# Performance work log

Measured on AMD Instinct MI355X. Metric: run time of the kernel, lower is better.

## Reference

```python
import jax, jax.numpy as jnp
import numpy as np

C, H_HEADS, L_LEV, M_PTS = 256, 4, 3, 4
TAU0 = 1.0


def _ln(x, g, b, eps=1e-5):
    mu = x.mean(-1, keepdims=True)
    var = ((x - mu) ** 2).mean(-1, keepdims=True)
    return (x - mu) * jax.lax.rsqrt(var + eps) * g + b


def _grid_sample(v, grid):
    """Bilinear grid_sample, padding_mode='zeros', align_corners=True.
    v: [B,C,Hin,Win], grid: [B,N,2] (x,y) in [-1,1] -> [B,N,C]"""
    B, Cc, Hin, Win = v.shape
    x = (grid[..., 0] + 1.0) * 0.5 * (Win - 1)
    y = (grid[..., 1] + 1.0) * 0.5 * (Hin - 1)
    x0 = jnp.floor(x); y0 = jnp.floor(y)
    wx1 = x - x0; wy1 = y - y0
    x0i = x0.astype(jnp.int32); y0i = y0.astype(jnp.int32)
    vflat = v.reshape(B, Cc, Hin * Win).transpose(0, 2, 1)  # [B,HW,C]

    def tap(yi, xi, w):
        valid = ((xi >= 0) & (xi < Win) & (yi >= 0) & (yi < Hin)).astype(v.dtype)
        idx = jnp.clip(yi, 0, Hin - 1) * Win + jnp.clip(xi, 0, Win - 1)  # [B,N]
        g = jax.vmap(lambda vf, i: vf[i])(vflat, idx)  # [B,N,C]
        return g * (w * valid)[..., None]

    return (tap(y0i, x0i, (1 - wy1) * (1 - wx1))
            + tap(y0i, x0i + 1, (1 - wy1) * wx1)
            + tap(y0i + 1, x0i, wy1 * (1 - wx1))
            + tap(y0i + 1, x0i + 1, wy1 * wx1))


def setup_inputs() -> dict:
    key = jax.random.key(0)
    ks = jax.random.split(key, 32)
    B, Hq, Wq = 2, 64, 64
    cins = [256, 512, 1024]
    d = {
        'S':  jax.random.normal(ks[0], (B, C, Hq, Wq), jnp.float32),
        'f0': jax.random.normal(ks[1], (B, cins[0], 64, 64), jnp.float32),
        'f1': jax.random.normal(ks[2], (B, cins[1], 32, 32), jnp.float32),
        'f2': jax.random.normal(ks[3], (B, cins[2], 16, 16), jnp.float32),
        'sim': jax.random.uniform(ks[4], (B, 1, Hq, Wq), jnp.float32),
        # 1x1 conv value projections per level
        'vw0': jax.random.normal(ks[5], (C, cins[0]), jnp.float32) * 0.02,
        'vb0': jnp.zeros((C,), jnp.float32),
        'vw1': jax.random.normal(ks[6], (C, cins[1]), jnp.float32) * 0.02,
        'vb1': jnp.zeros((C,), jnp.float32),
        'vw2': jax.random.normal(ks[7], (C, cins[2]), jnp.float32) * 0.02,
        'vb2': jnp.zeros((C,), jnp.float32),
        'q_w': jax.random.normal(ks[8], (C, C), jnp.float32) * 0.02,
        'q_b': jnp.zeros((C,), jnp.float32),
        # offset/weight predictors (non-zero so sampling is nontrivial)
        'off_w': jax.random.normal(ks[9], (H_HEADS * L_LEV * M_PTS * 2, C), jnp.float32) * 0.01,
        'off_b': jnp.zeros((H_HEADS * L_LEV * M_PTS * 2,), jnp.float32),
        'wgt_w': jax.random.normal(ks[10], (H_HEADS * L_LEV * M_PTS, C), jnp.float32) * 0.02,
        'wgt_b': jnp.zeros((H_HEADS * L_LEV * M_PTS,), jnp.float32),
        'out_w': jax.random.normal(ks[11], (C, H_HEADS * C), jnp.float32) * 0.02,
        'out_b': jnp.zeros((C,), jnp.float32),
        'lnq_g': jnp.ones((C,), jnp.float32), 'lnq_b': jnp.zeros((C,), jnp.float32),
        'lno_g': jnp.ones((C,), jnp.float32), 'lno_b': jnp.zeros((C,), jnp.float32),
        'fc1_w': jax.random.normal(ks[12], (4 * C, C), jnp.float32) * 0.02,
        'fc1_b': jnp.zeros((4 * C,), jnp.float32),
        'fc2_w': jax.random.normal(ks[13], (C, 4 * C), jnp.float32) * 0.02,
        'fc2_b': jnp.zeros((C,), jnp.float32),
    }
    return d


def reference(S, f0, f1, f2, sim, vw0, vb0, vw1, vb1, vw2, vb2, q_w, q_b,
              off_w, off_b, wgt_w, wgt_b, out_w, out_b,
              lnq_g, lnq_b, lno_g, lno_b, fc1_w, fc1_b, fc2_w, fc2_b):
    B, Cc, Hq, Wq = S.shape
    Nq = Hq * Wq
    S_seq = S.reshape(B, Cc, Nq).transpose(0, 2, 1)  # [B,Nq,C]
    Q = _ln(S_seq @ q_w.T + q_b, lnq_g, lnq_b)

    # reference points in [0,1], (x,y)
    ys = jnp.linspace(0.5 / Hq, 1 - 0.5 / Hq, Hq)
    xs = jnp.linspace(0.5 / Wq, 1 - 0.5 / Wq, Wq)
    yy, xx = jnp.meshgrid(ys, xs, indexing='ij')
    ref = jnp.stack([xx, yy], axis=-1).reshape(1, Nq, 2)

    feats = [(f0, vw0, vb0), (f1, vw1, vb1), (f2, vw2, vb2)]
    V = [jnp.einsum('bchw,oc->bohw', f, w) + b[None, :, None, None] for f, w, b in feats]

    off = (Q @ off_w.T + off_b).reshape(B, Nq, H_HEADS, L_LEV, M_PTS, 2)
    wts = (Q @ wgt_w.T + wgt_b).reshape(B, Nq, H_HEADS, L_LEV, M_PTS)

    sim2 = sim[:, 0].reshape(B, Nq, 1)
    tau = TAU0 / (sim2 + 0.001)
    wts = wts / tau.reshape(B, Nq, 1, 1, 1)
    wts = jax.nn.softmax(wts.reshape(B, Nq, H_HEADS, L_LEV * M_PTS), axis=-1)
    wts = wts.reshape(B, Nq, H_HEADS, L_LEV, M_PTS)

    acc = jnp.zeros((B, Nq, H_HEADS, Cc), S.dtype)
    for l in range(L_LEV):
        g01 = ref.reshape(1, Nq, 1, 1, 2) + off[:, :, :, l]  # [B,Nq,H,M,2]
        g = jnp.clip(jnp.tanh(g01 * 2.0 - 1.0), -1.0, 1.0)
        samp = _grid_sample(V[l], g.reshape(B, Nq * H_HEADS * M_PTS, 2))
        samp = samp.reshape(B, Nq, H_HEADS, M_PTS, Cc)
        acc = acc + jnp.einsum('bqhmc,bqhm->bqhc', samp, wts[:, :, :, l])

    Y = acc.reshape(B, Nq, H_HEADS * Cc) @ out_w.T + out_b
    Z = _ln(S_seq + Y, lno_g, lno_b)
    h = jax.nn.gelu(Z @ fc1_w.T + fc1_b, approximate=False)
    Z = Z + (h @ fc2_w.T + fc2_b)
    return Z.transpose(0, 2, 1).reshape(B, Cc, Hq, Wq)
```

## Files before the change

### kernel.cpp

```cpp
#include <hip/hip_runtime.h>
#include <hip/hip_bf16.h>
#include <math.h>

#define NQ 4096
#define CC 256

typedef __attribute__((ext_vector_type(8))) short bfrag;
typedef __attribute__((ext_vector_type(4))) float ffrag;

__device__ inline unsigned short f2bf(float x) {
  __hip_bfloat16 h = __float2bfloat16(x);
  return *reinterpret_cast<unsigned short*>(&h);
}

__device__ inline void gload16(const void* g, void* l) {
  __builtin_amdgcn_global_load_lds(
      (const __attribute__((address_space(1))) void*)g,
      (__attribute__((address_space(3))) void*)l, 16, 0, 0);
}

__device__ void tr64(const float* __restrict__ src,
                     unsigned short* __restrict__ dstb, int Cin, int P,
                     int p0, int c0, int b, float (*t)[73]) {
  int tid = threadIdx.x;
  int rx = tid & 15, ry = tid >> 4;
  const float* Sb = src + (size_t)b * Cin * P + p0 + rx * 4;
  #pragma unroll
  for (int i = 0; i < 4; i++) {
    int r = ry + i * 16;
    float4 v = *(const float4*)(Sb + (size_t)(c0 + r) * P);
    t[r][rx * 4 + 0] = v.x; t[r][rx * 4 + 1] = v.y;
    t[r][rx * 4 + 2] = v.z; t[r][rx * 4 + 3] = v.w;
  }
  __syncthreads();
  size_t ob = (size_t)b * P * Cin;
  #pragma unroll
  for (int i = 0; i < 4; i++) {
    int pr = ry + i * 16;
    float x0 = t[rx * 4 + 0][pr], x1 = t[rx * 4 + 1][pr];
    float x2 = t[rx * 4 + 2][pr], x3 = t[rx * 4 + 3][pr];
    size_t idx = ob + (size_t)(p0 + pr) * Cin + c0 + rx * 4;
    ushort4 u4;
    u4.x = f2bf(x0); u4.y = f2bf(x1); u4.z = f2bf(x2); u4.w = f2bf(x3);
    *(ushort4*)(dstb + idx) = u4;
  }
}

__global__ __launch_bounds__(256)
void prep_all_k(const float* S, const float* f0, const float* f1, const float* f2,
                const float* q_w, const float* off_w, const float* wgt_w,
                const float* vw0, const float* vw1, const float* vw2,
                const float* out_w, const float* fc1_w, const float* fc2_w,
                const float* off_b, const float* wgt_b,
                unsigned short* Sbf,
                unsigned short* Xf0, unsigned short* Xf1, unsigned short* Xf2,
                unsigned short* q_wb, unsigned short* owb,
                unsigned short* vw0b, unsigned short* vw1b, unsigned short* vw2b,
                unsigned short* out_wb, unsigned short* fc1_wb,
                unsigned short* fc2_wb, float* bias144) {
  __shared__ float t[64][73];
  int bid = blockIdx.x;
  if (bid < 512) {
    int l = bid;
    tr64(S, Sbf, 256, 4096, (l & 63) * 64, ((l >> 6) & 3) * 64, l >> 8, t);
  } else if (bid < 1024) {
    int l = bid - 512;
    tr64(f0, Xf0, 256, 4096, (l & 63) * 64, ((l >> 6) & 3) * 64, l >> 8, t);
  } else if (bid < 1280) {
    int l = bid - 1024;
    tr64(f1, Xf1, 512, 1024, (l & 15) * 64, ((l >> 4) & 7) * 64, l >> 7, t);
  } else if (bid < 1408) {
    int l = bid - 1280;
    tr64(f2, Xf2, 1024, 256, (l & 3) * 64, ((l >> 2) & 15) * 64, l >> 6, t);
  } else if (bid < 2688) {
    int i4 = (bid - 1408) * 256 + threadIdx.x;
    const float* src; unsigned short* dst;
    if (i4 < 16384)       { src = q_w;   dst = q_wb; }
    else if (i4 < 32768)  { i4 -= 16384;  src = vw0;   dst = vw0b; }
    else if (i4 < 65536)  { i4 -= 32768;  src = vw1;   dst = vw1b; }
    else if (i4 < 131072) { i4 -= 65536;  src = vw2;   dst = vw2b; }
    else if (i4 < 196608) { i4 -= 131072; src = out_w; dst = out_wb; }
    else if (i4 < 262144) { i4 -= 196608; src = fc1_w; dst = fc1_wb; }
    else                  { i4 -= 262144; src = fc2_w; dst = fc2_wb; }
    float4 v = ((const float4*)src)[i4];
    ushort4 u; u.x = f2bf(v.x); u.y = f2bf(v.y); u.z = f2bf(v.z); u.w = f2bf(v.w);
    ((ushort4*)dst)[i4] = u;
  } else {
    int e = (bid - 2688) * 256 + threadIdx.x;
    float v = (e < 24576) ? off_w[e] : (e < 36864 ? wgt_w[e - 24576] : 0.f);
    owb[e] = f2bf(v);
    if (e < 96) bias144[e] = off_b[e];
    else if (e < 144) bias144[e] = wgt_b[e - 96];
  }
}

template<int BM, int BN, int WM, int WN, int EPI>
__device__ __forceinline__ void gemm_body(
    const unsigned short* __restrict__ A, const unsigned short* __restrict__ B,
    const float* __restrict__ bias, float* __restrict__ outf,
    unsigned short* __restrict__ outb, int N, int Kloop, int lda, int ldb,
    int ldo, int m0, int n0, unsigned short* As, unsigned short* Bs) {
  constexpr int MI = BM / (WM * 16), NI = BN / (WN * 16);
  constexpr int TA = BM / 8, TB = BN / 8;
  constexpr int LBM = (BM == 32) ? 5 : (BM == 64) ? 6 : 7;
  constexpr int LBN = (BN == 64) ? 6 : (BN == 128) ? 7 : 8;
  int tid = threadIdx.x, wave = tid >> 6, lane = tid & 63;
  int quad = lane >> 4, l16 = lane & 15;
  int wm = wave / WN, wn = wave % WN;
  const int mbase = wm * (BM / WM), nbase = wn * (BN / WN);

  ffrag acc[MI][NI];
  #pragma unroll
  for (int i = 0; i < MI; i++)
    #pragma unroll
    for (int j = 0; j < NI; j++) acc[i][j] = (ffrag)0.f;

  for (int k0 = 0; k0 < Kloop; k0 += 64) {
    __syncthreads();
    for (int t = wave; t < TA + TB; t += 4) {
      if (t < TA) {
        int s = t * 64 + lane;
        int kc = s >> LBM, r = s & (BM - 1);
        gload16(A + (size_t)(m0 + r) * lda + k0 + kc * 8, (char*)As + t * 1024);
      } else {
        int s = (t - TA) * 64 + lane;
        int kc = s >> LBN, r = s & (BN - 1);
        gload16(B + (size_t)(n0 + r) * ldb + k0 + kc * 8, (char*)Bs + (t - TA) * 1024);
      }
    }
    __syncthreads();
    #pragma unroll
    for (int ks = 0; ks < 2; ks++) {
      bfrag af[MI], bf[NI];
      #pragma unroll
      for (int mi = 0; mi < MI; mi++)
        af[mi] = *(const bfrag*)(As + ((((ks * 4 + quad) << LBM) + mbase + mi * 16 + l16) << 3));
      #pragma unroll
      for (int ni = 0; ni < NI; ni++)
        bf[ni] = *(const bfrag*)(Bs + ((((ks * 4 + quad) << LBN) + nbase + ni * 16 + l16) << 3));
      #pragma unroll
      for (int mi = 0; mi < MI; mi++)
        #pragma unroll
        for (int ni = 0; ni < NI; ni++)
          acc[mi][ni] = __builtin_amdgcn_mfma_f32_16x16x32_bf16(
              af[mi], bf[ni], acc[mi][ni], 0, 0, 0);
    }
  }

  #pragma unroll
  for (int mi = 0; mi < MI; mi++) {
    int mrow = m0 + mbase + mi * 16 + quad * 4;
    #pragma unroll
    for (int ni = 0; ni < NI; ni++) {
      int n = n0 + nbase + ni * 16 + l16;
      if (n < N) {
        float bv = (EPI == 4) ? 0.f : bias[n];
        #pragma unroll
        for (int r = 0; r < 4; r++) {
          float v = acc[mi][ni][r] + bv;
          if (EPI == 1) {
            v = 0.5f * v * (1.f + erff(v * 0.70710678118654752f));
            outb[(size_t)(mrow + r) * ldo + n] = f2bf(v);
          } else if (EPI == 3) {
            outb[(size_t)(mrow + r) * ldo + n] = f2bf(v);
          } else {
            outf[(size_t)(mrow + r) * ldo + n] = v;
          }
        }
      }
    }
  }
}

__device__ __forceinline__ void gemm_ln_q(
    const unsigned short* __restrict__ A, const unsigned short* __restrict__ B,
    const float* __restrict__ bias, unsigned short* __restrict__ outb,
    const float* __restrict__ g, const float* __restrict__ be,
    int m0, char* sm) {
  unsigned short* As = (unsigned short*)sm;
  unsigned short* Bs = (unsigned short*)(sm + 4096);
  float* L = (float*)sm;
  const int K = 256;

  int tid = threadIdx.x, wave = tid >> 6, lane = tid & 63;
  int quad = lane >> 4, l16 = lane & 15;

  ffrag acc[2][4];
  #pragma unroll
  for (int i = 0; i < 2; i++)
    #pragma unroll
    for (int j = 0; j < 4; j++) acc[i][j] = (ffrag)0.f;

  for (int k0 = 0; k0 < K; k0 += 64) {
    __syncthreads();
    for (int t = wave; t < 36; t += 4) {
      if (t < 4) {
        int s = t * 64 + lane;
        int kc = s >> 5, r = s & 31;
        gload16(A + (size_t)(m0 + r) * K + k0 + kc * 8, sm + t * 1024);
      } else {
        int s = (t - 4) * 64 + lane;
        int kc = s >> 8, r = s & 255;
        gload16(B + (size_t)r * K + k0 + kc * 8, sm + 4096 + (t - 4) * 1024);
      }
    }
    __syncthreads();
    #pragma unroll
    for (int ks = 0; ks < 2; ks++) {
      bfrag af[2], bf[4];
      #pragma unroll
      for (int mi = 0; mi < 2; mi++)
        af[mi] = *(const bfrag*)(As + ((((ks * 4 + quad) << 5) + mi * 16 + l16) << 3));
      #pragma unroll
      for (int ni = 0; ni < 4; ni++)
        bf[ni] = *(const bfrag*)(Bs + ((((ks * 4 + quad) << 8) + wave * 64 + ni * 16 + l16) << 3));
      #pragma unroll
      for (int mi = 0; mi < 2; mi++)
        #pragma unroll
        for (int ni = 0; ni < 4; ni++)
          acc[mi][ni] = __builtin_amdgcn_mfma_f32_16x16x32_bf16(
              af[mi], bf[ni], acc[mi][ni], 0, 0, 0);
    }
  }
  __syncthreads();

  #pragma unroll
  for (int mi = 0; mi < 2; mi++) {
    int row = mi * 16 + quad * 4;
    #pragma unroll
    for (int ni = 0; ni < 4; ni++) {
      int col = wave * 64 + ni * 16 + l16;
      float bv = bias[col];
      #pragma unroll
      for (int r = 0; r < 4; r++)
        L[(row + r) * 264 + col] = acc[mi][ni][r] + bv;
    }
  }
  __syncthreads();

  int row = tid >> 3, j = tid & 7;
  int seg = ((j + row) & 7) * 32;
  const float* Lr = L + row * 264 + seg;
  float s1 = 0.f, s2 = 0.f;
  #pragma unroll
  for (int i = 0; i < 8; i++) {
    float4 t4 = *(const float4*)(Lr + i * 4);
    s1 += t4.x + t4.y + t4.z + t4.w;
    s2 += t4.x * t4.x + t4.y * t4.y + t4.z * t4.z + t4.w * t4.w;
  }
  #pragma unroll
  for (int o = 1; o < 8; o <<= 1) {
    s1 += __shfl_xor(s1, o);
    s2 += __shfl_xor(s2, o);
  }
  float mu = s1 * (1.f / 256.f);
  float var = s2 * (1.f / 256.f) - mu * mu;
  float rs = rsqrtf(var + 1e-5f);
  int gm = m0 + row;
  #pragma unroll
  for (int i = 0; i < 8; i++) {
    int col = seg + i * 4;
    float4 t4 = *(const float4*)(Lr + i * 4);
    float4 gg = *(const float4*)(g + col);
    float4 bb4 = *(const float4*)(be + col);
    ushort4 ub;
    ub.x = f2bf((t4.x - mu) * rs * gg.x + bb4.x);
    ub.y = f2bf((t4.y - mu) * rs * gg.y + bb4.y);
    ub.z = f2bf((t4.z - mu) * rs * gg.z + bb4.z);
    ub.w = f2bf((t4.w - mu) * rs * gg.w + bb4.w);
    *(ushort4*)(outb + (size_t)gm * CC + col) = ub;
  }
}

__global__ __launch_bounds__(256)
void qv_k(const unsigned short* Sbf, const unsigned short* q_wb, const float* q_b,
          const float* lnq_g, const float* lnq_b, unsigned short* Qbf,
          const unsigned short* Xf0, const unsigned short* Xf1,
          const unsigned short* Xf2, const unsigned short* vw0b,
          const unsigned short* vw1b, const unsigned short* vw2b,
          const float* vb0, unsigned short* V0b, float* Vp1, float* Vp2) {
  __shared__ __attribute__((aligned(16))) char sm[36864];
  int bid = blockIdx.x;
  unsigned short* As = (unsigned short*)sm;
  unsigned short* Bs = (unsigned short*)(sm + 8192);
  if (bid < 256) {
    gemm_ln_q(Sbf, q_wb, q_b, Qbf, lnq_g, lnq_b, bid * 32, sm);
  } else if (bid < 512) {
    int t = bid - 256;
    gemm_body<64, 128, 2, 2, 3>(Xf0, vw0b, vb0, nullptr, V0b, 256, 256, 256, 256,
                                256, (t >> 1) * 64, (t & 1) * 128, As, Bs);
  } else if (bid < 640) {
    int l = bid - 512, ks = l >> 6, t = l & 63;
    gemm_body<64, 128, 2, 2, 4>(Xf1 + ks * 256, vw1b + ks * 256, nullptr,
                                Vp1 + (size_t)ks * 524288, nullptr, 256, 256, 512, 512,
                                256, (t >> 1) * 64, (t & 1) * 128, As, Bs);
  } else {
    int l = bid - 640, ks = l >> 4, t = l & 15;
    gemm_body<64, 128, 2, 2, 4>(Xf2 + ks * 256, vw2b + ks * 256, nullptr,
                                Vp2 + (size_t)ks * 131072, nullptr, 256, 256, 1024, 1024,
                                256, (t >> 1) * 64, (t & 1) * 128, As, Bs);
  }
}

__global__ __launch_bounds__(256)
void offv_k(const unsigned short* Qbf, const unsigned short* owb,
            const float* bias144, float* offwgt,
            const float* Vp1, const float* Vp2, const float* vb1,
            const float* vb2, unsigned short* V1b, unsigned short* V2b) {
  __shared__ __attribute__((aligned(16))) unsigned short As[4096];
  __shared__ __attribute__((aligned(16))) unsigned short Bs[8192];
  int bid = blockIdx.x;
  if (bid < 256) {
    gemm_body<64, 128, 2, 2, 0>(Qbf, owb, bias144, offwgt, nullptr, 144, 256, 256,
                                256, 144, (bid >> 1) * 64, (bid & 1) * 128, As, Bs);
  } else if (bid < 768) {
    int e4 = (bid - 256) * 256 + threadIdx.x;
    const float4* P = (const float4*)Vp1;
    float4 a = P[e4], b = P[e4 + 131072];
    float4 bb = *(const float4*)(vb1 + ((e4 << 2) & 255));
    ushort4 u;
    u.x = f2bf(a.x + b.x + bb.x); u.y = f2bf(a.y + b.y + bb.y);
    u.z = f2bf(a.z + b.z + bb.z); u.w = f2bf(a.w + b.w + bb.w);
    ((ushort4*)V1b)[e4] = u;
  } else {
    int e4 = (bid - 768) * 256 + threadIdx.x;
    const float4* P = (const float4*)Vp2;
    float4 a = P[e4], b = P[e4 + 32768], c = P[e4 + 65536], d = P[e4 + 98304];
    float4 bb = *(const float4*)(vb2 + ((e4 << 2) & 255));
    ushort4 u;
    u.x = f2bf(a.x + b.x + c.x + d.x + bb.x);
    u.y = f2bf(a.y + b.y + c.y + d.y + bb.y);
    u.z = f2bf(a.z + b.z + c.z + d.z + bb.z);
    u.w = f2bf(a.w + b.w + c.w + d.w + bb.w);
    ((ushort4*)V2b)[e4] = u;
  }
}

__global__ __launch_bounds__(256)
void outA_k(const unsigned short* accbf, const unsigned short* out_wb, float* Op) {
  __shared__ __attribute__((aligned(16))) char sm[36864];
  int ks = blockIdx.y;
  gemm_body<32, 256, 1, 4, 4>(accbf + ks * 256, out_wb + ks * 256, nullptr,
                              Op + (size_t)ks * 2097152, nullptr, 256, 256, 1024,
                              1024, 256, blockIdx.x * 32, 0,
                              (unsigned short*)sm, (unsigned short*)(sm + 4096));
}

__global__ __launch_bounds__(256)
void outB_k(const float* __restrict__ Op, const float* __restrict__ S,
            const float* __restrict__ out_b, const float* __restrict__ g,
            const float* __restrict__ be, float* __restrict__ Zf,
            unsigned short* __restrict__ Zbf) {
  __shared__ float Ls[16][264];
  int q0 = blockIdx.x * 16;
  int b = q0 >> 12, qq = q0 & (NQ - 1);
  int t = threadIdx.x;
  {
    int cs = t >> 2, j = (t & 3) * 4;
    #pragma unroll
    for (int c0 = 0; c0 < 256; c0 += 64) {
      float4 sv = *(const float4*)(S + (((size_t)(b * 256 + c0 + cs)) << 12) + qq + j);
      Ls[j + 0][c0 + cs] = sv.x; Ls[j + 1][c0 + cs] = sv.y;
      Ls[j + 2][c0 + cs] = sv.z; Ls[j + 3][c0 + cs] = sv.w;
    }
  }
  __syncthreads();
  int c = t;
  float bv = out_b[c];
  float val[16];
  #pragma unroll
  for (int r = 0; r < 16; r++) {
    size_t idx = (size_t)(q0 + r) * 256 + c;
    val[r] = Op[idx] + Op[idx + 2097152] + Op[idx + 4194304] + Op[idx + 6291456]
           + bv + Ls[r][c];
  }
  __syncthreads();
  #pragma unroll
  for (int r = 0; r < 16; r++) Ls[r][c] = val[r];
  __syncthreads();
  int row = t >> 4, lg = t & 15;
  const float* Lr = &Ls[row][lg * 16];
  float s1 = 0.f, s2 = 0.f;
  #pragma unroll
  for (int i = 0; i < 4; i++) {
    float4 t4 = *(const float4*)(Lr + i * 4);
    s1 += t4.x + t4.y + t4.z + t4.w;
    s2 += t4.x * t4.x + t4.y * t4.y + t4.z * t4.z + t4.w * t4.w;
  }
  #pragma unroll
  for (int o = 1; o < 16; o <<= 1) {
    s1 += __shfl_xor(s1, o);
    s2 += __shfl_xor(s2, o);
  }
  float mu = s1 * (1.f / 256.f);
  float var = s2 * (1.f / 256.f) - mu * mu;
  float rs = rsqrtf(var + 1e-5f);
  int gm = q0 + row;
  #pragma unroll
  for (int i = 0; i < 4; i++) {
    int col = lg * 16 + i * 4;
    float4 t4 = *(const float4*)(Lr + i * 4);
    float4 gg = *(const float4*)(g + col);
    float4 bb4 = *(const float4*)(be + col);
    float4 y;
    y.x = (t4.x - mu) * rs * gg.x + bb4.x;
    y.y = (t4.y - mu) * rs * gg.y + bb4.y;
    y.z = (t4.z - mu) * rs * gg.z + bb4.z;
    y.w = (t4.w - mu) * rs * gg.w + bb4.w;
    *(float4*)(Zf + (size_t)gm * CC + col) = y;
    ushort4 ub;
    ub.x = f2bf(y.x); ub.y = f2bf(y.y); ub.z = f2bf(y.z); ub.w = f2bf(y.w);
    *(ushort4*)(Zbf + (size_t)gm * CC + col) = ub;
  }
}

__global__ __launch_bounds__(256)
void fc1_k(const unsigned short* Zbf, const unsigned short* fc1_wb,
           const float* fc1_b, unsigned short* hbf) {
  __shared__ __attribute__((aligned(16))) unsigned short As[4096];
  __shared__ __attribute__((aligned(16))) unsigned short Bs[8192];
  gemm_body<64, 128, 2, 2, 1>(Zbf, fc1_wb, fc1_b, nullptr, hbf, 1024, 256, 256,
                              256, 1024, blockIdx.y * 64, blockIdx.x * 128, As, Bs);
}

__global__ __launch_bounds__(256)
void fc2A_k(const unsigned short* hbf, const unsigned short* fc2_wb, float* Fp) {
  __shared__ __attribute__((aligned(16))) char sm[36864];
  int ks = blockIdx.y;
  gemm_body<32, 256, 1, 4, 4>(hbf + ks * 256, fc2_wb + ks * 256, nullptr,
                              Fp + (size_t)ks * 2097152, nullptr, 256, 256, 1024,
                              1024, 256, blockIdx.x * 32, 0,
                              (unsigned short*)sm, (unsigned short*)(sm + 4096));
}

__global__ __launch_bounds__(256)
void fc2B_k(const float* __restrict__ Fp, const float* __restrict__ Z,
            const float* __restrict__ fc2_b, float* __restrict__ outp) {
  int q0 = blockIdx.x * 64;
  int b = q0 >> 12, qq = q0 & (NQ - 1);
  int n = threadIdx.x;
  float bv = fc2_b[n];
  float* od = outp + (((size_t)(b * 256 + n)) << 12) + qq;
  #pragma unroll
  for (int g4 = 0; g4 < 16; g4++) {
    float4 o;
    #pragma unroll
    for (int j = 0; j < 4; j++) {
      size_t idx = (size_t)(q0 + g4 * 4 + j) * 256 + n;
      float v = Fp[idx] + Fp[idx + 2097152] + Fp[idx + 4194304] + Fp[idx + 6291456]
              + Z[idx] + bv;
      ((float*)&o)[j] = v;
    }
    *(float4*)(od + g4 * 4) = o;
  }
}

__global__ __launch_bounds__(256)
void sample_k(const float* __restrict__ ow, const float* __restrict__ sim,
              const unsigned short* __restrict__ V0, const unsigned short* __restrict__ V1,
              const unsigned short* __restrict__ V2, unsigned short* __restrict__ acc) {
  int bn = blockIdx.x;
  int q = ((bn & 7) << 10) | (bn >> 3);
  int b = q >> 12, n = q & (NQ - 1);
  int tid = threadIdx.x, head = tid >> 6, lane = tid & 63;
  int half = lane >> 5, l32 = lane & 31;

  __shared__ float s_w[48];
  __shared__ int   s_xy[48][2];
  __shared__ float s_f[48][2];
  __shared__ uint2 s_ow[192];

  if (tid < 48) {
    int hh = tid / 12, pt = tid % 12, l = pt >> 2, mm = pt & 3;
    int oidx = (hh * 3 + l) * 4 + mm;
    float offx = ow[(size_t)q * 144 + oidx * 2 + 0];
    float offy = ow[(size_t)q * 144 + oidx * 2 + 1];
    float refx = ((n & 63) + 0.5f) * (1.f / 64.f);
    float refy = ((n >> 6) + 0.5f) * (1.f / 64.f);
    float gx = tanhf((refx + offx) * 2.f - 1.f);
    float gy = tanhf((refy + offy) * 2.f - 1.f);
    gx = fminf(1.f, fmaxf(-1.f, gx));
    gy = fminf(1.f, fmaxf(-1.f, gy));
    int Wl = 64 >> l;
    float x = (gx + 1.f) * 0.5f * (float)(Wl - 1);
    float y = (gy + 1.f) * 0.5f * (float)(Wl - 1);
    float x0 = floorf(x), y0 = floorf(y);
    s_xy[tid][0] = (int)x0;
    s_xy[tid][1] = (int)y0;
    s_f[tid][0] = x - x0;
    s_f[tid][1] = y - y0;
    s_w[tid] = ow[(size_t)q * 144 + 96 + oidx] * (sim[q] + 0.001f);
  }
  __syncthreads();
  if (tid < 4) {
    float mx = -1e30f;
    #pragma unroll
    for (int i = 0; i < 12; i++) mx = fmaxf(mx, s_w[tid * 12 + i]);
    float e[12], ssum = 0.f;
    #pragma unroll
    for (int i = 0; i < 12; i++) { e[i] = expf(s_w[tid * 12 + i] - mx); ssum += e[i]; }
    float inv = 1.f / ssum;
    #pragma unroll
    for (int i = 0; i < 12; i++) s_w[tid * 12 + i] = e[i] * inv;
  }
  __syncthreads();
  if (tid < 192) {
    int s = tid >> 2, tap = tid & 3;
    int l = (s % 12) >> 2;
    int Wl = 64 >> l;
    int X = s_xy[s][0] + (tap & 1), Y = s_xy[s][1] + (tap >> 1);
    bool valid = (X >= 0 && X < Wl && Y >= 0 && Y < Wl);
    float wx = (tap & 1) ? s_f[s][0] : 1.f - s_f[s][0];
    float wy = (tap >> 1) ? s_f[s][1] : 1.f - s_f[s][1];
    float twt = valid ? s_w[s] * wx * wy : 0.f;
    int Xc = min(max(X, 0), Wl - 1), Yc = min(max(Y, 0), Wl - 1);
    s_ow[tid].x = (unsigned)((Yc * Wl + Xc) << 8);
    s_ow[tid].y = __float_as_uint(twt);
  }
  __syncthreads();

  const unsigned short* B0 = V0 + (size_t)b * 4096 * CC;
  const unsigned short* B1 = V1 + (size_t)b * 1024 * CC;
  const unsigned short* B2 = V2 + (size_t)b * 256 * CC;
  int ch8 = l32 * 8;
  float a0 = 0.f, a1 = 0.f, a2 = 0.f, a3 = 0.f;
  float a4 = 0.f, a5 = 0.f, a6 = 0.f, a7 = 0.f;
  #pragma unroll
  for (int it = 0; it < 24; it++) {
    const unsigned short* base = (it < 8) ? B0 : (it < 16) ? B1 : B2;
    uint2 owv = s_ow[head * 48 + it * 2 + half];
    float w = __uint_as_float(owv.y);
    const uint4 u = *(const uint4*)(base + owv.x + ch8);
    a0 = fmaf(w, __uint_as_float(u.x << 16), a0);
    a1 = fmaf(w, __uint_as_float(u.x & 0xffff0000u), a1);
    a2 = fmaf(w, __uint_as_float(u.y << 16), a2);
    a3 = fmaf(w, __uint_as_float(u.y & 0xffff0000u), a3);
    a4 = fmaf(w, __uint_as_float(u.z << 16), a4);
    a5 = fmaf(w, __uint_as_float(u.z & 0xffff0000u), a5);
    a6 = fmaf(w, __uint_as_float(u.w << 16), a6);
    a7 = fmaf(w, __uint_as_float(u.w & 0xffff0000u), a7);
  }
  a0 += __shfl_xor(a0, 32); a1 += __shfl_xor(a1, 32);
  a2 += __shfl_xor(a2, 32); a3 += __shfl_xor(a3, 32);
  a4 += __shfl_xor(a4, 32); a5 += __shfl_xor(a5, 32);
  a6 += __shfl_xor(a6, 32); a7 += __shfl_xor(a7, 32);
  if (half == 0) {
    uint4 r;
    r.x = (unsigned)f2bf(a0) | ((unsigned)f2bf(a1) << 16);
    r.y = (unsigned)f2bf(a2) | ((unsigned)f2bf(a3) << 16);
    r.z = (unsigned)f2bf(a4) | ((unsigned)f2bf(a5) << 16);
    r.w = (unsigned)f2bf(a6) | ((unsigned)f2bf(a7) << 16);
    *(uint4*)(acc + (size_t)q * 1024 + head * CC + ch8) = r;
  }
}

extern "C" void kernel_launch(void* const* d_in, const int* in_sizes, int n_in,
                              void* d_out, int out_size, void* d_ws, size_t ws_size,
                              hipStream_t stream) {
  const float* S     = (const float*)d_in[0];
  const float* f0    = (const float*)d_in[1];
  const float* f1    = (const float*)d_in[2];
  const float* f2    = (const float*)d_in[3];
  const float* sim   = (const float*)d_in[4];
  const float* vw0   = (const float*)d_in[5];
  const float* vb0   = (const float*)d_in[6];
  const float* vw1   = (const float*)d_in[7];
  const float* vb1   = (const float*)d_in[8];
  const float* vw2   = (const float*)d_in[9];
  const float* vb2   = (const float*)d_in[10];
  const float* q_w   = (const float*)d_in[11];
  const float* q_b   = (const float*)d_in[12];
  const float* off_w = (const float*)d_in[13];
  const float* off_b = (const float*)d_in[14];
  const float* wgt_w = (const float*)d_in[15];
  const float* wgt_b = (const float*)d_in[16];
  const float* out_w = (const float*)d_in[17];
  const float* out_b = (const float*)d_in[18];
  const float* lnq_g = (const float*)d_in[19];
  const float* lnq_b = (const float*)d_in[20];
  const float* lno_g = (const float*)d_in[21];
  const float* lno_b = (const float*)d_in[22];
  const float* fc1_w = (const float*)d_in[23];
  const float* fc1_b = (const float*)d_in[24];
  const float* fc2_w = (const float*)d_in[25];
  const float* fc2_b = (const float*)d_in[26];

  char* p = (char*)d_ws;
  float* Z      = (float*)p; p += 8388608;
  float* offwgt = (float*)p; p += 4718592;
  float* bias144 = (float*)p; p += 1024;
  float* Pp     = (float*)p; p += 33554432;
  float* Vp1    = (float*)p; p += 4194304;
  float* Vp2    = (float*)p; p += 2097152;
  unsigned short* Sbf   = (unsigned short*)p; p += 4194304;
  unsigned short* Qbf   = (unsigned short*)p; p += 4194304;
  unsigned short* accbf = (unsigned short*)p; p += 16777216;
  unsigned short* V0b   = (unsigned short*)p; p += 4194304;
  unsigned short* V1b   = (unsigned short*)p; p += 1048576;
  unsigned short* V2b   = (unsigned short*)p; p += 262144;
  unsigned short* q_wb   = (unsigned short*)p; p += 131072;
  unsigned short* owb    = (unsigned short*)p; p += 131072;
  unsigned short* vw0b   = (unsigned short*)p; p += 131072;
  unsigned short* vw1b   = (unsigned short*)p; p += 262144;
  unsigned short* vw2b   = (unsigned short*)p; p += 524288;
  unsigned short* out_wb = (unsigned short*)p; p += 524288;
  unsigned short* fc1_wb = (unsigned short*)p; p += 524288;
  unsigned short* fc2_wb = (unsigned short*)p; p += 524288;

  unsigned short* Xf0 = accbf;
  unsigned short* Xf1 = accbf + 2097152;
  unsigned short* Xf2 = accbf + 3145728;
  unsigned short* Zbf = Qbf;
  unsigned short* hbf = accbf;
  float* outp = (float*)d_out;

  prep_all_k<<<2944, 256, 0, stream>>>(S, f0, f1, f2, q_w, off_w, wgt_w,
      vw0, vw1, vw2, out_w, fc1_w, fc2_w, off_b, wgt_b,
      Sbf, Xf0, Xf1, Xf2, q_wb, owb, vw0b, vw1b, vw2b, out_wb,
      fc1_wb, fc2_wb, bias144);

  qv_k<<<704, 256, 0, stream>>>(Sbf, q_wb, q_b, lnq_g, lnq_b, Qbf,
      Xf0, Xf1, Xf2, vw0b, vw1b, vw2b, vb0, V0b, Vp1, Vp2);

  offv_k<<<896, 256, 0, stream>>>(Qbf, owb, bias144, offwgt,
      Vp1, Vp2, vb1, vb2, V1b, V2b);

  sample_k<<<8192, 256, 0, stream>>>(offwgt, sim, V0b, V1b, V2b, accbf);

  outA_k<<<dim3(256, 4), 256, 0, stream>>>(accbf, out_wb, Pp);

  outB_k<<<512, 256, 0, stream>>>(Pp, S, out_b, lno_g, lno_b, Z, Zbf);

  fc1_k<<<dim3(8, 128), 256, 0, stream>>>(Zbf, fc1_wb, fc1_b, hbf);

  fc2A_k<<<dim3(256, 4), 256, 0, stream>>>(hbf, fc2_wb, Pp);

  fc2B_k<<<128, 256, 0, stream>>>(Pp, Z, fc2_b, outp);
}
```

Baseline: 286.5 us.

## Fuse fc2 split-K GEMM and reduction into single full-K GEMM with transposed epilogue

Replaces the split-K fc2 GEMM (4 partial outputs) plus a separate reduction kernel with a single 64x64-tile GEMM over the full K=1024. A new epilogue adds bias and the Z residual and writes the result transposed to the [B,C,H,W] layout with float4 stores. This removes the 32 MB partial-sum round trip and one launch, but gives 512 blocks each looping over a longer K instead of 1024 shorter ones.

```diff
diff --git a/kernel.cpp b/kernel.cpp
--- a/kernel.cpp
+++ b/kernel.cpp
@@ -99,7 +99,8 @@
     const unsigned short* __restrict__ A, const unsigned short* __restrict__ B,
     const float* __restrict__ bias, float* __restrict__ outf,
     unsigned short* __restrict__ outb, int N, int Kloop, int lda, int ldb,
-    int ldo, int m0, int n0, unsigned short* As, unsigned short* Bs) {
+    int ldo, const float* __restrict__ Zres, float* __restrict__ outT,
+    int m0, int n0, unsigned short* As, unsigned short* Bs) {
   constexpr int MI = BM / (WM * 16), NI = BN / (WN * 16);
   constexpr int TA = BM / 8, TB = BN / 8;
   constexpr int LBM = (BM == 32) ? 5 : (BM == 64) ? 6 : 7;
@@ -147,24 +148,43 @@
     }
   }
 
-  #pragma unroll
-  for (int mi = 0; mi < MI; mi++) {
-    int mrow = m0 + mbase + mi * 16 + quad * 4;
-    #pragma unroll
-    for (int ni = 0; ni < NI; ni++) {
-      int n = n0 + nbase + ni * 16 + l16;
-      if (n < N) {
-        float bv = (EPI == 4) ? 0.f : bias[n];
-        #pragma unroll
-        for (int r = 0; r < 4; r++) {
-          float v = acc[mi][ni][r] + bv;
-          if (EPI == 1) {
-            v = 0.5f * v * (1.f + erff(v * 0.70710678118654752f));
-            outb[(size_t)(mrow + r) * ldo + n] = f2bf(v);
-          } else if (EPI == 3) {
-            outb[(size_t)(mrow + r) * ldo + n] = f2bf(v);
-          } else {
-            outf[(size_t)(mrow + r) * ldo + n] = v;
+  if (EPI == 2) {
+    #pragma unroll
+    for (int mi = 0; mi < MI; mi++) {
+      int mrow = m0 + mbase + mi * 16 + quad * 4;
+      int bb = mrow >> 12, q0 = mrow & (NQ - 1);
+      #pragma unroll
+      for (int ni = 0; ni < NI; ni++) {
+        int n = n0 + nbase + ni * 16 + l16;
+        float bv = bias[n];
+        float4 v;
+        v.x = acc[mi][ni][0] + bv + Zres[(size_t)(mrow + 0) * CC + n];
+        v.y = acc[mi][ni][1] + bv + Zres[(size_t)(mrow + 1) * CC + n];
+        v.z = acc[mi][ni][2] + bv + Zres[(size_t)(mrow + 2) * CC + n];
+        v.w = acc[mi][ni][3] + bv + Zres[(size_t)(mrow + 3) * CC + n];
+        *(float4*)(outT + ((size_t)(bb * CC + n)) * NQ + q0) = v;
+      }
+    }
+  } else {
+    #pragma unroll
+    for (int mi = 0; mi < MI; mi++) {
+      int mrow = m0 + mbase + mi * 16 + quad * 4;
+      #pragma unroll
+      for (int ni = 0; ni < NI; ni++) {
+        int n = n0 + nbase + ni * 16 + l16;
+        if (n < N) {
+          float bv = (EPI == 4) ? 0.f : bias[n];
+          #pragma unroll
+          for (int r = 0; r < 4; r++) {
+            float v = acc[mi][ni][r] + bv;
+            if (EPI == 1) {
+              v = 0.5f * v * (1.f + erff(v * 0.70710678118654752f));
+              outb[(size_t)(mrow + r) * ldo + n] = f2bf(v);
+            } else if (EPI == 3) {
+              outb[(size_t)(mrow + r) * ldo + n] = f2bf(v);
+            } else {
+              outf[(size_t)(mrow + r) * ldo + n] = v;
+            }
           }
         }
       }
@@ -288,17 +308,17 @@
   } else if (bid < 512) {
     int t = bid - 256;
     gemm_body<64, 128, 2, 2, 3>(Xf0, vw0b, vb0, nullptr, V0b, 256, 256, 256, 256,
-                                256, (t >> 1) * 64, (t & 1) * 128, As, Bs);
+                                256, nullptr, nullptr, (t >> 1) * 64, (t & 1) * 128, As, Bs);
   } else if (bid < 640) {
     int l = bid - 512, ks = l >> 6, t = l & 63;
     gemm_body<64, 128, 2, 2, 4>(Xf1 + ks * 256, vw1b + ks * 256, nullptr,
                                 Vp1 + (size_t)ks * 524288, nullptr, 256, 256, 512, 512,
-                                256, (t >> 1) * 64, (t & 1) * 128, As, Bs);
+                                256, nullptr, nullptr, (t >> 1) * 64, (t & 1) * 128, As, Bs);
   } else {
     int l = bid - 640, ks = l >> 4, t = l & 15;
     gemm_body<64, 128, 2, 2, 4>(Xf2 + ks * 256, vw2b + ks * 256, nullptr,
                                 Vp2 + (size_t)ks * 131072, nullptr, 256, 256, 1024, 1024,
-                                256, (t >> 1) * 64, (t & 1) * 128, As, Bs);
+                                256, nullptr, nullptr, (t >> 1) * 64, (t & 1) * 128, As, Bs);
   }
 }
 
@@ -312,7 +332,8 @@
   int bid = blockIdx.x;
   if (bid < 256) {
     gemm_body<64, 128, 2, 2, 0>(Qbf, owb, bias144, offwgt, nullptr, 144, 256, 256,
-                                256, 144, (bid >> 1) * 64, (bid & 1) * 128, As, Bs);
+                                256, 144, nullptr, nullptr,
+                                (bid >> 1) * 64, (bid & 1) * 128, As, Bs);
   } else if (bid < 768) {
     int e4 = (bid - 256) * 256 + threadIdx.x;
     const float4* P = (const float4*)Vp1;
@@ -342,7 +363,7 @@
   int ks = blockIdx.y;
   gemm_body<32, 256, 1, 4, 4>(accbf + ks * 256, out_wb + ks * 256, nullptr,
                               Op + (size_t)ks * 2097152, nullptr, 256, 256, 1024,
-                              1024, 256, blockIdx.x * 32, 0,
+                              1024, 256, nullptr, nullptr, blockIdx.x * 32, 0,
                               (unsigned short*)sm, (unsigned short*)(sm + 4096));
 }
 
@@ -420,39 +441,18 @@
   __shared__ __attribute__((aligned(16))) unsigned short As[4096];
   __shared__ __attribute__((aligned(16))) unsigned short Bs[8192];
   gemm_body<64, 128, 2, 2, 1>(Zbf, fc1_wb, fc1_b, nullptr, hbf, 1024, 256, 256,
-                              256, 1024, blockIdx.y * 64, blockIdx.x * 128, As, Bs);
-}
-
-__global__ __launch_bounds__(256)
-void fc2A_k(const unsigned short* hbf, const unsigned short* fc2_wb, float* Fp) {
-  __shared__ __attribute__((aligned(16))) char sm[36864];
-  int ks = blockIdx.y;
-  gemm_body<32, 256, 1, 4, 4>(hbf + ks * 256, fc2_wb + ks * 256, nullptr,
-                              Fp + (size_t)ks * 2097152, nullptr, 256, 256, 1024,
-                              1024, 256, blockIdx.x * 32, 0,
-                              (unsigned short*)sm, (unsigned short*)(sm + 4096));
-}
-
-__global__ __launch_bounds__(256)
-void fc2B_k(const float* __restrict__ Fp, const float* __restrict__ Z,
-            const float* __restrict__ fc2_b, float* __restrict__ outp) {
-  int q0 = blockIdx.x * 64;
-  int b = q0 >> 12, qq = q0 & (NQ - 1);
-  int n = threadIdx.x;
-  float bv = fc2_b[n];
-  float* od = outp + (((size_t)(b * 256 + n)) << 12) + qq;
-  #pragma unroll
-  for (int g4 = 0; g4 < 16; g4++) {
-    float4 o;
-    #pragma unroll
-    for (int j = 0; j < 4; j++) {
-      size_t idx = (size_t)(q0 + g4 * 4 + j) * 256 + n;
-      float v = Fp[idx] + Fp[idx + 2097152] + Fp[idx + 4194304] + Fp[idx + 6291456]
-              + Z[idx] + bv;
-      ((float*)&o)[j] = v;
-    }
-    *(float4*)(od + g4 * 4) = o;
-  }
+                              256, 1024, nullptr, nullptr,
+                              blockIdx.y * 64, blockIdx.x * 128, As, Bs);
+}
+
+__global__ __launch_bounds__(256)
+void fc2_k(const unsigned short* hbf, const unsigned short* fc2_wb,
+           const float* fc2_b, const float* Z, float* outp) {
+  __shared__ __attribute__((aligned(16))) unsigned short As[4096];
+  __shared__ __attribute__((aligned(16))) unsigned short Bs[4096];
+  gemm_body<64, 64, 2, 2, 2>(hbf, fc2_wb, fc2_b, nullptr, nullptr, 256, 1024,
+                             1024, 1024, 256, Z, outp,
+                             blockIdx.y * 64, blockIdx.x * 64, As, Bs);
 }
 
 __global__ __launch_bounds__(256)
@@ -633,7 +633,5 @@
 
   fc1_k<<<dim3(8, 128), 256, 0, stream>>>(Zbf, fc1_wb, fc1_b, hbf);
 
-  fc2A_k<<<dim3(256, 4), 256, 0, stream>>>(hbf, fc2_wb, Pp);
-
-  fc2B_k<<<128, 256, 0, stream>>>(Pp, Z, fc2_b, outp);
-}
+  fc2_k<<<dim3(4, 128), 256, 0, stream>>>(hbf, fc2_wb, fc2_b, Z, outp);
+}
```

Measured after the change: 269.1 us. -6.1%, faster.
